# Kernel optimization log

Hardware: AMD Instinct MI355X
Metric: run time of the kernel (lower is better)

Reference implementation:

```python
import jax, jax.numpy as jnp
import numpy as np

B, S, D, H = 2, 2048, 1024, 16
DK = D // H


def setup_inputs() -> dict:
    key = jax.random.key(0)
    ks = jax.random.split(key, 12)
    scale = 1.0 / np.sqrt(D)
    inp = {
        "q": jax.random.normal(ks[0], (B, S, D), dtype=jnp.float32),
        "k": jax.random.normal(ks[1], (B, S, D), dtype=jnp.float32),
        "v": jax.random.normal(ks[2], (B, S, D), dtype=jnp.float32),
        "mask": jax.random.randint(ks[3], (B, 1, 1, S), 0, 2, dtype=jnp.int32),
        "Wq": jax.random.normal(ks[4], (D, D), dtype=jnp.float32) * scale,
        "bq": jnp.zeros((D,), dtype=jnp.float32),
        "Wk": jax.random.normal(ks[5], (D, D), dtype=jnp.float32) * scale,
        "bk": jnp.zeros((D,), dtype=jnp.float32),
        "Wv": jax.random.normal(ks[6], (D, D), dtype=jnp.float32) * scale,
        "bv": jnp.zeros((D,), dtype=jnp.float32),
        "Wo": jax.random.normal(ks[7], (D, D), dtype=jnp.float32) * scale,
        "bo": jnp.zeros((D,), dtype=jnp.float32),
    }
    return inp


def reference(q, k, v, mask, Wq, bq, Wk, bk, Wv, bv, Wo, bo):
    # Linear projections (torch nn.Linear: x @ W.T + b)
    query = q @ Wq.T + bq                      # [B,S,D]
    key = k @ Wk.T + bk
    value = v @ Wv.T + bv
    # split heads -> [B,H,S,DK]
    def split(x):
        return x.reshape(B, S, H, DK).transpose(0, 2, 1, 3)
    qh, kh, vh = split(query), split(key), split(value)
    # scaled dot-product attention with additive mask
    scores = jnp.einsum("bhqd,bhkd->bhqk", qh, kh) / jnp.sqrt(jnp.float32(DK))
    scores = jnp.where(mask == 0, jnp.float32(-1e9), scores)
    attn = jax.nn.softmax(scores, axis=-1)     # [B,H,S,S]
    out = jnp.einsum("bhqk,bhkd->bhqd", attn, vh)
    out = out.transpose(0, 2, 1, 3).reshape(B, S, D)
    return out @ Wo.T + bo
```

## Files before the change

kernel.cpp:

```cpp
#include <hip/hip_runtime.h>


constexpr int BB = 2;
constexpr int SS = 2048;
constexpr int DD = 1024;
constexpr int HH = 16;
constexpr int DKK = 64;

typedef float f32x4 __attribute__((ext_vector_type(4)));
typedef __bf16 bf16x8 __attribute__((ext_vector_type(8)));
typedef short s16x8 __attribute__((ext_vector_type(8)));
typedef short s16x4 __attribute__((ext_vector_type(4)));

#define DEV static __device__ __forceinline__

DEV f32x4 mfma16(s16x8 a, s16x8 b, f32x4 c) {
  return __builtin_amdgcn_mfma_f32_16x16x32_bf16(
      __builtin_bit_cast(bf16x8, a), __builtin_bit_cast(bf16x8, b), c, 0, 0, 0);
}

DEV void split1(float x, short& h, short& l) {
  unsigned u = __float_as_uint(x);
  h = (short)(u >> 16);
  float hf = __uint_as_float(u & 0xffff0000u);
  l = (short)(__float_as_uint(x - hf) >> 16);
}
DEV short f2bf_rne(float x) {
  unsigned u = __float_as_uint(x);
  return (short)((u + 0x7fffu + ((u >> 16) & 1u)) >> 16);
}
DEV s16x8 load8s(const short* p) { return *(const s16x8*)p; }

DEV void gld_lds16(const short* g, short* l) {
  __builtin_amdgcn_global_load_lds(
      (const __attribute__((address_space(1))) void*)g,
      (__attribute__((address_space(3))) void*)l, 16, 0, 0);
}

__global__ __launch_bounds__(256) void split_pair(const float* __restrict__ X,
                                                  short* __restrict__ H,
                                                  short* __restrict__ L) {
  int i = (blockIdx.x * 256 + threadIdx.x) * 4;
  float4 x = *(const float4*)(X + i);
  float xs[4] = {x.x, x.y, x.z, x.w};
  s16x4 h4, l4;
#pragma unroll
  for (int e = 0; e < 4; ++e) {
    short h, l;
    split1(xs[e], h, l);
    h4[e] = h;
    l4[e] = l;
  }
  *(s16x4*)(H + i) = h4;
  *(s16x4*)(L + i) = l4;
}

__global__ __launch_bounds__(256) void cast_rne(const float* __restrict__ X,
                                                short* __restrict__ Y) {
  int i = (blockIdx.x * 256 + threadIdx.x) * 4;
  float4 x = *(const float4*)(X + i);
  float xs[4] = {x.x, x.y, x.z, x.w};
  s16x4 y4;
#pragma unroll
  for (int e = 0; e < 4; ++e) y4[e] = f2bf_rne(xs[e]);
  *(s16x4*)(Y + i) = y4;
}

__global__ __launch_bounds__(256) void gemm_qk(
    const short* __restrict__ qAh, const short* __restrict__ qAl,
    const short* __restrict__ Wqh, const short* __restrict__ Wql,
    const float* __restrict__ bq, short* __restrict__ Qo,
    const short* __restrict__ kAh, const short* __restrict__ kAl,
    const short* __restrict__ Wkh, const short* __restrict__ Wkl,
    const float* __restrict__ bk, short* __restrict__ Kho,
    short* __restrict__ Klo) {
  __shared__ short lds[2][12288];

  const int tid = threadIdx.x;
  const int lane = tid & 63, wv = tid >> 6;
  const int lo16 = lane & 15, quad = lane >> 4;
  const int sel = blockIdx.x >> 9;
  const int bid = blockIdx.x & 511;
  const int m0 = (bid & 31) * 128;
  const int n0 = (bid >> 5) * 64;

  const short* Agh = sel ? kAh : qAh;
  const short* Agl = sel ? kAl : qAl;
  const short* Wgh = sel ? Wkh : Wqh;
  const short* Wgl = sel ? Wkl : Wql;
  const float* bias = sel ? bk : bq;

  f32x4 acc[2][4];
#pragma unroll
  for (int mt = 0; mt < 2; ++mt)
#pragma unroll
    for (int nt = 0; nt < 4; ++nt) acc[mt][nt] = f32x4{0.f, 0.f, 0.f, 0.f};

  const int rw = tid >> 2, qw = tid & 3;
  const int ra0 = tid >> 2, ra1 = (tid + 256) >> 2;

  auto stage = [&](int k0, int buf) {
    short* sAh = lds[buf];
    short* sAl = lds[buf] + 4096;
    short* sWh = lds[buf] + 8192;
    short* sWl = lds[buf] + 10240;
    gld_lds16(Wgh + (size_t)(n0 + rw) * DD + k0 + qw * 8, sWh + tid * 8);
    gld_lds16(Wgl + (size_t)(n0 + rw) * DD + k0 + qw * 8, sWl + tid * 8);
    gld_lds16(Agh + (size_t)(m0 + ra0) * DD + k0 + qw * 8, sAh + tid * 8);
    gld_lds16(Agh + (size_t)(m0 + ra1) * DD + k0 + qw * 8, sAh + (tid + 256) * 8);
    gld_lds16(Agl + (size_t)(m0 + ra0) * DD + k0 + qw * 8, sAl + tid * 8);
    gld_lds16(Agl + (size_t)(m0 + ra1) * DD + k0 + qw * 8, sAl + (tid + 256) * 8);
  };

  stage(0, 0);

  for (int kk = 0; kk < DD / 32; ++kk) {
    __syncthreads();
    if (kk + 1 < DD / 32) stage((kk + 1) * 32, (kk + 1) & 1);

    const short* sAh = lds[kk & 1];
    const short* sAl = lds[kk & 1] + 4096;
    const short* sWh = lds[kk & 1] + 8192;
    const short* sWl = lds[kk & 1] + 10240;

    s16x8 ah[2], al[2], wh[4], wl[4];
#pragma unroll
    for (int mt = 0; mt < 2; ++mt) {
      const int r = wv * 32 + mt * 16 + lo16;
      ah[mt] = *(const s16x8*)&sAh[r * 32 + quad * 8];
      al[mt] = *(const s16x8*)&sAl[r * 32 + quad * 8];
    }
#pragma unroll
    for (int nt = 0; nt < 4; ++nt) {
      const int r = nt * 16 + lo16;
      wh[nt] = *(const s16x8*)&sWh[r * 32 + quad * 8];
      wl[nt] = *(const s16x8*)&sWl[r * 32 + quad * 8];
    }
#pragma unroll
    for (int mt = 0; mt < 2; ++mt)
#pragma unroll
      for (int nt = 0; nt < 4; ++nt) {
        acc[mt][nt] = mfma16(ah[mt], wh[nt], acc[mt][nt]);
        acc[mt][nt] = mfma16(ah[mt], wl[nt], acc[mt][nt]);
        acc[mt][nt] = mfma16(al[mt], wh[nt], acc[mt][nt]);
      }
  }

#pragma unroll
  for (int mt = 0; mt < 2; ++mt)
#pragma unroll
    for (int nt = 0; nt < 4; ++nt) {
      const int n = n0 + nt * 16 + lo16;
      const float bv = bias[n];
#pragma unroll
      for (int r = 0; r < 4; ++r) {
        const int m = m0 + wv * 32 + mt * 16 + quad * 4 + r;
        const float val = acc[mt][nt][r] + bv;
        const int b = m >> 11, s = m & 2047;
        const int h = n >> 6, dk = n & 63;
        size_t idx = ((size_t)(b * HH + h) * SS + s) * DKK + dk;
        if (sel == 0) {
          Qo[idx] = f2bf_rne(val);
        } else {
          short hh, ll;
          split1(val, hh, ll);
          Kho[idx] = hh;
          Klo[idx] = ll;
        }
      }
    }
}

template <int SPLIT, int EPI>
__global__ __launch_bounds__(256) void gemm_tile(
    const short* __restrict__ Agh, const short* __restrict__ Agl,
    const short* __restrict__ Wgh, const short* __restrict__ Wgl,
    const float* __restrict__ bias, void* __restrict__ O1, void* __restrict__ O2) {
  __shared__ short lds[2][12288];

  const int tid = threadIdx.x;
  const int lane = tid & 63, wv = tid >> 6;
  const int lo16 = lane & 15, quad = lane >> 4;
  const int m0 = (blockIdx.x & 31) * 128;
  const int n0 = (blockIdx.x >> 5) * 64;

  f32x4 acc[2][4];
#pragma unroll
  for (int mt = 0; mt < 2; ++mt)
#pragma unroll
    for (int nt = 0; nt < 4; ++nt) acc[mt][nt] = f32x4{0.f, 0.f, 0.f, 0.f};

  const int rw = tid >> 2, qw = tid & 3;
  const int ra0 = tid >> 2, ra1 = (tid + 256) >> 2;

  auto stage = [&](int k0, int buf) {
    short* sAh = lds[buf];
    short* sAl = lds[buf] + 4096;
    short* sWh = lds[buf] + 8192;
    short* sWl = lds[buf] + 10240;
    gld_lds16(Wgh + (size_t)(n0 + rw) * DD + k0 + qw * 8, sWh + tid * 8);
    if constexpr (SPLIT)
      gld_lds16(Wgl + (size_t)(n0 + rw) * DD + k0 + qw * 8, sWl + tid * 8);
    gld_lds16(Agh + (size_t)(m0 + ra0) * DD + k0 + qw * 8, sAh + tid * 8);
    gld_lds16(Agh + (size_t)(m0 + ra1) * DD + k0 + qw * 8, sAh + (tid + 256) * 8);
    if constexpr (SPLIT) {
      gld_lds16(Agl + (size_t)(m0 + ra0) * DD + k0 + qw * 8, sAl + tid * 8);
      gld_lds16(Agl + (size_t)(m0 + ra1) * DD + k0 + qw * 8, sAl + (tid + 256) * 8);
    }
  };

  stage(0, 0);

  for (int kk = 0; kk < DD / 32; ++kk) {
    __syncthreads();
    if (kk + 1 < DD / 32) stage((kk + 1) * 32, (kk + 1) & 1);

    const short* sAh = lds[kk & 1];
    const short* sAl = lds[kk & 1] + 4096;
    const short* sWh = lds[kk & 1] + 8192;
    const short* sWl = lds[kk & 1] + 10240;

    s16x8 ah[2], al[2], wh[4], wl[4];
#pragma unroll
    for (int mt = 0; mt < 2; ++mt) {
      const int r = wv * 32 + mt * 16 + lo16;
      ah[mt] = *(const s16x8*)&sAh[r * 32 + quad * 8];
      if constexpr (SPLIT) al[mt] = *(const s16x8*)&sAl[r * 32 + quad * 8];
    }
#pragma unroll
    for (int nt = 0; nt < 4; ++nt) {
      const int r = nt * 16 + lo16;
      wh[nt] = *(const s16x8*)&sWh[r * 32 + quad * 8];
      if constexpr (SPLIT) wl[nt] = *(const s16x8*)&sWl[r * 32 + quad * 8];
    }
#pragma unroll
    for (int mt = 0; mt < 2; ++mt)
#pragma unroll
      for (int nt = 0; nt < 4; ++nt) {
        acc[mt][nt] = mfma16(ah[mt], wh[nt], acc[mt][nt]);
        if constexpr (SPLIT) {
          acc[mt][nt] = mfma16(ah[mt], wl[nt], acc[mt][nt]);
          acc[mt][nt] = mfma16(al[mt], wh[nt], acc[mt][nt]);
        }
      }
  }

#pragma unroll
  for (int mt = 0; mt < 2; ++mt)
#pragma unroll
    for (int nt = 0; nt < 4; ++nt) {
      const int n = n0 + nt * 16 + lo16;
      const float bv = bias[n];
#pragma unroll
      for (int r = 0; r < 4; ++r) {
        const int m = m0 + wv * 32 + mt * 16 + quad * 4 + r;
        const float val = acc[mt][nt][r] + bv;
        const int b = m >> 11, s = m & 2047;
        const int h = n >> 6, dk = n & 63;
        if constexpr (EPI == 1) {
          size_t idx = ((size_t)(b * HH + h) * DKK + dk) * SS + s;
          ((short*)O1)[idx] = f2bf_rne(val);
        } else {
          ((float*)O1)[(size_t)m * DD + n] = val;
        }
      }
    }
}

constexpr int PAD = 68;
constexpr int NKB = SS / 64;

__global__ __launch_bounds__(256, 2) void mha_attn(
    const short* __restrict__ Qh, const short* __restrict__ Kh,
    const short* __restrict__ Kl, const short* __restrict__ Vt,
    const int* __restrict__ mask, short* __restrict__ Ah,
    short* __restrict__ Al) {
  __shared__ short sKh[64 * PAD];
  __shared__ short sKl[64 * PAD];
  __shared__ short sV[64 * PAD];
  __shared__ short sP[4][32 * PAD];

  const int tid = threadIdx.x;
  const int lane = tid & 63, wv = tid >> 6;
  const int lo16 = lane & 15, quad = lane >> 4;
  const int bid = blockIdx.x;
  const int head = (bid & 7) * 4 + ((bid >> 3) & 3);
  const int qblk = bid >> 5;
  const int q0 = qblk * 128 + wv * 32;
  const int b = head >> 4;

  const size_t hbase = (size_t)head * SS;

  s16x8 qh[2][2];
#pragma unroll
  for (int rt = 0; rt < 2; ++rt) {
    size_t qb = (hbase + q0 + rt * 16 + lo16) * DKK + quad * 8;
#pragma unroll
    for (int c = 0; c < 2; ++c) qh[rt][c] = load8s(Qh + qb + c * 32);
  }

  f32x4 Oacc[2][4];
#pragma unroll
  for (int rt = 0; rt < 2; ++rt)
#pragma unroll
    for (int t = 0; t < 4; ++t) Oacc[rt][t] = f32x4{0.f, 0.f, 0.f, 0.f};
  float lsum[2][4];
#pragma unroll
  for (int rt = 0; rt < 2; ++rt)
#pragma unroll
    for (int r = 0; r < 4; ++r) lsum[rt][r] = 0.f;

  const int srow = tid >> 2;
  const int scol0 = (tid & 3) * 8;

  s16x8 rKh[2], rKl[2], rV[2];
#pragma unroll
  for (int i = 0; i < 2; ++i) {
    const int sc_ = scol0 + i * 32;
    rKh[i] = load8s(Kh + (hbase + srow) * DKK + sc_);
    rKl[i] = load8s(Kl + (hbase + srow) * DKK + sc_);
    rV[i] = load8s(Vt + ((size_t)head * DKK + srow) * SS + sc_);
  }

  for (int kb = 0; kb < NKB; ++kb) {
    const int k0g = kb * 64;
#pragma unroll
    for (int i = 0; i < 2; ++i) {
      const int sc_ = scol0 + i * 32;
      *(s16x8*)&sKh[srow * PAD + sc_] = rKh[i];
      *(s16x8*)&sKl[srow * PAD + sc_] = rKl[i];
      *(s16x8*)&sV[srow * PAD + sc_] = rV[i];
    }
    __syncthreads();

    if (kb + 1 < NKB) {
      const int k0n = k0g + 64;
#pragma unroll
      for (int i = 0; i < 2; ++i) {
        const int sc_ = scol0 + i * 32;
        rKh[i] = load8s(Kh + (hbase + k0n + srow) * DKK + sc_);
        rKl[i] = load8s(Kl + (hbase + k0n + srow) * DKK + sc_);
        rV[i] = load8s(Vt + ((size_t)head * DKK + srow) * SS + k0n + sc_);
      }
    }

    f32x4 sc4[2][4];
    int mv[4];
#pragma unroll
    for (int sub = 0; sub < 4; ++sub) {
      mv[sub] = mask[b * SS + k0g + sub * 16 + lo16];
      sc4[0][sub] = f32x4{0.f, 0.f, 0.f, 0.f};
      sc4[1][sub] = f32x4{0.f, 0.f, 0.f, 0.f};
      const int krow = sub * 16 + lo16;
#pragma unroll
      for (int c = 0; c < 2; ++c) {
        s16x8 kh = *(const s16x8*)&sKh[krow * PAD + c * 32 + quad * 8];
        s16x8 kl = *(const s16x8*)&sKl[krow * PAD + c * 32 + quad * 8];
#pragma unroll
        for (int rt = 0; rt < 2; ++rt) {
          sc4[rt][sub] = mfma16(qh[rt][c], kh, sc4[rt][sub]);
          sc4[rt][sub] = mfma16(qh[rt][c], kl, sc4[rt][sub]);
        }
      }
    }

#pragma unroll
    for (int rt = 0; rt < 2; ++rt)
#pragma unroll
      for (int sub = 0; sub < 4; ++sub)
#pragma unroll
        for (int r = 0; r < 4; ++r) {
          float p = __expf(sc4[rt][sub][r] * 0.125f);
          p = mv[sub] ? p : 0.f;
          lsum[rt][r] += p;
          sP[wv][(rt * 16 + quad * 4 + r) * PAD + sub * 16 + lo16] = f2bf_rne(p);
        }

    s16x8 pa[2][2];
#pragma unroll
    for (int rt = 0; rt < 2; ++rt)
#pragma unroll
      for (int c = 0; c < 2; ++c)
        pa[rt][c] = *(const s16x8*)&sP[wv][(rt * 16 + lo16) * PAD + c * 32 + quad * 8];
#pragma unroll
    for (int t = 0; t < 4; ++t)
#pragma unroll
      for (int c = 0; c < 2; ++c) {
        s16x8 vb = *(const s16x8*)&sV[(t * 16 + lo16) * PAD + c * 32 + quad * 8];
#pragma unroll
        for (int rt = 0; rt < 2; ++rt)
          Oacc[rt][t] = mfma16(pa[rt][c], vb, Oacc[rt][t]);
      }
    __syncthreads();
  }

  const int h = head & 15;
#pragma unroll
  for (int rt = 0; rt < 2; ++rt)
#pragma unroll
    for (int r = 0; r < 4; ++r) {
      float s = lsum[rt][r];
#pragma unroll
      for (int off = 1; off < 16; off <<= 1) s += __shfl_xor(s, off);
      const float rinv = 1.0f / s;
#pragma unroll
      for (int t = 0; t < 4; ++t) {
        const float val = Oacc[rt][t][r] * rinv;
        const int row = q0 + rt * 16 + quad * 4 + r;
        const int col = h * DKK + t * 16 + lo16;
        const size_t idx = ((size_t)b * SS + row) * DD + col;
        short hh, ll;
        split1(val, hh, ll);
        Ah[idx] = hh;
        Al[idx] = ll;
      }
    }
}

extern "C" void kernel_launch(void* const* d_in, const int* in_sizes, int n_in,
                              void* d_out, int out_size, void* d_ws, size_t ws_size,
                              hipStream_t stream) {
  const float* q = (const float*)d_in[0];
  const float* k = (const float*)d_in[1];
  const float* v = (const float*)d_in[2];
  const int* mask = (const int*)d_in[3];
  const float* Wq = (const float*)d_in[4];
  const float* bq = (const float*)d_in[5];
  const float* Wk = (const float*)d_in[6];
  const float* bk = (const float*)d_in[7];
  const float* Wv = (const float*)d_in[8];
  const float* bv = (const float*)d_in[9];
  const float* Wo = (const float*)d_in[10];
  const float* bo = (const float*)d_in[11];

  char* ws = (char*)d_ws;
  size_t off = 0;
  auto take = [&](size_t bytes) {
    char* p = ws + off;
    off += (bytes + 255) & ~(size_t)255;
    return p;
  };
  const size_t WE = (size_t)DD * DD;
  const size_t TE = (size_t)BB * SS * DD;

  short* Wqh = (short*)take(WE * 2);
  short* Wql = (short*)take(WE * 2);
  short* Wkh = (short*)take(WE * 2);
  short* Wkl = (short*)take(WE * 2);
  short* Wvh = (short*)take(WE * 2);
  short* Woh = (short*)take(WE * 2);
  short* Wol = (short*)take(WE * 2);
  short* qH = (short*)take(TE * 2);
  short* qL = (short*)take(TE * 2);
  short* kH = (short*)take(TE * 2);
  short* kL = (short*)take(TE * 2);
  short* Qh = (short*)take(TE * 2);
  short* Kh = (short*)take(TE * 2);
  short* Kl = (short*)take(TE * 2);
  (void)ws_size;
  short* vH = qH;
  short* Vt = qL;
  short* aH = kH;
  short* aL = kL;

  split_pair<<<1024, 256, 0, stream>>>(Wq, Wqh, Wql);
  split_pair<<<1024, 256, 0, stream>>>(Wk, Wkh, Wkl);
  split_pair<<<1024, 256, 0, stream>>>(Wo, Woh, Wol);
  cast_rne<<<1024, 256, 0, stream>>>(Wv, Wvh);

  split_pair<<<4096, 256, 0, stream>>>(q, qH, qL);
  split_pair<<<4096, 256, 0, stream>>>(k, kH, kL);

  gemm_qk<<<1024, 256, 0, stream>>>(qH, qL, Wqh, Wql, bq, Qh,
                                    kH, kL, Wkh, Wkl, bk, Kh, Kl);

  cast_rne<<<4096, 256, 0, stream>>>(v, vH);
  gemm_tile<0, 1><<<512, 256, 0, stream>>>(vH, nullptr, Wvh, nullptr, bv, Vt, nullptr);

  mha_attn<<<512, 256, 0, stream>>>(Qh, Kh, Kl, Vt, mask, aH, aL);

  gemm_tile<1, 2><<<512, 256, 0, stream>>>(aH, aL, Woh, Wol, bo, d_out, nullptr);
}
```

Measured before the change: 332.2 us.

## Load GEMM A operands directly to registers and swizzle W LDS tiles

In both projection GEMM kernels, the A-operand fragments are now loaded straight from global memory into registers with one-step register prefetch, since each wave owns its own A rows and needs no LDS sharing. Only the W tiles are staged through double-buffered LDS, which shrinks shared memory per block from 48KB to 16KB. W tiles use an XOR swizzle of the 8-element column chunks to reduce LDS bank conflicts on the MFMA fragment reads. The trade-off is more live registers and uncoalesced-ish per-lane global loads of A, in exchange for higher occupancy and less LDS traffic.

```diff
diff --git a/kernel.cpp b/kernel.cpp
--- a/kernel.cpp
+++ b/kernel.cpp
@@ -74,7 +74,7 @@
     const short* __restrict__ Wkh, const short* __restrict__ Wkl,
     const float* __restrict__ bk, short* __restrict__ Kho,
     short* __restrict__ Klo) {
-  __shared__ short lds[2][12288];
+  __shared__ short lds[2][4096];
 
   const int tid = threadIdx.x;
   const int lane = tid & 63, wv = tid >> 6;
@@ -96,45 +96,41 @@
 #pragma unroll
     for (int nt = 0; nt < 4; ++nt) acc[mt][nt] = f32x4{0.f, 0.f, 0.f, 0.f};
 
-  const int rw = tid >> 2, qw = tid & 3;
-  const int ra0 = tid >> 2, ra1 = (tid + 256) >> 2;
-
-  auto stage = [&](int k0, int buf) {
-    short* sAh = lds[buf];
-    short* sAl = lds[buf] + 4096;
-    short* sWh = lds[buf] + 8192;
-    short* sWl = lds[buf] + 10240;
-    gld_lds16(Wgh + (size_t)(n0 + rw) * DD + k0 + qw * 8, sWh + tid * 8);
-    gld_lds16(Wgl + (size_t)(n0 + rw) * DD + k0 + qw * 8, sWl + tid * 8);
-    gld_lds16(Agh + (size_t)(m0 + ra0) * DD + k0 + qw * 8, sAh + tid * 8);
-    gld_lds16(Agh + (size_t)(m0 + ra1) * DD + k0 + qw * 8, sAh + (tid + 256) * 8);
-    gld_lds16(Agl + (size_t)(m0 + ra0) * DD + k0 + qw * 8, sAl + tid * 8);
-    gld_lds16(Agl + (size_t)(m0 + ra1) * DD + k0 + qw * 8, sAl + (tid + 256) * 8);
-  };
-
-  stage(0, 0);
+  const int wr = tid >> 2, wp = tid & 3;
+  const size_t wsrc = (size_t)(n0 + wr) * DD + (wp ^ ((wr >> 1) & 3)) * 8;
+  const int pq = quad ^ ((lo16 >> 1) & 3);
+
+  const size_t a0 = (size_t)(m0 + wv * 32 + lo16) * DD + quad * 8;
+  const size_t a1 = a0 + (size_t)16 * DD;
+
+  s16x8 ah[2], al[2];
+  ah[0] = load8s(Agh + a0);
+  ah[1] = load8s(Agh + a1);
+  al[0] = load8s(Agl + a0);
+  al[1] = load8s(Agl + a1);
+  gld_lds16(Wgh + wsrc, &lds[0][tid * 8]);
+  gld_lds16(Wgl + wsrc, &lds[0][2048 + tid * 8]);
 
   for (int kk = 0; kk < DD / 32; ++kk) {
     __syncthreads();
-    if (kk + 1 < DD / 32) stage((kk + 1) * 32, (kk + 1) & 1);
-
-    const short* sAh = lds[kk & 1];
-    const short* sAl = lds[kk & 1] + 4096;
-    const short* sWh = lds[kk & 1] + 8192;
-    const short* sWl = lds[kk & 1] + 10240;
-
-    s16x8 ah[2], al[2], wh[4], wl[4];
-#pragma unroll
-    for (int mt = 0; mt < 2; ++mt) {
-      const int r = wv * 32 + mt * 16 + lo16;
-      ah[mt] = *(const s16x8*)&sAh[r * 32 + quad * 8];
-      al[mt] = *(const s16x8*)&sAl[r * 32 + quad * 8];
-    }
+    s16x8 ahn[2], aln[2];
+    const bool more = (kk + 1 < DD / 32);
+    if (more) {
+      const int k1 = (kk + 1) * 32;
+      gld_lds16(Wgh + wsrc + k1, &lds[(kk + 1) & 1][tid * 8]);
+      gld_lds16(Wgl + wsrc + k1, &lds[(kk + 1) & 1][2048 + tid * 8]);
+      ahn[0] = load8s(Agh + a0 + k1);
+      ahn[1] = load8s(Agh + a1 + k1);
+      aln[0] = load8s(Agl + a0 + k1);
+      aln[1] = load8s(Agl + a1 + k1);
+    }
+    const short* sWh = lds[kk & 1];
+    const short* sWl = lds[kk & 1] + 2048;
+    s16x8 wh[4], wl[4];
 #pragma unroll
     for (int nt = 0; nt < 4; ++nt) {
-      const int r = nt * 16 + lo16;
-      wh[nt] = *(const s16x8*)&sWh[r * 32 + quad * 8];
-      wl[nt] = *(const s16x8*)&sWl[r * 32 + quad * 8];
+      wh[nt] = *(const s16x8*)&sWh[(nt * 16 + lo16) * 32 + pq * 8];
+      wl[nt] = *(const s16x8*)&sWl[(nt * 16 + lo16) * 32 + pq * 8];
     }
 #pragma unroll
     for (int mt = 0; mt < 2; ++mt)
@@ -144,6 +140,12 @@
         acc[mt][nt] = mfma16(ah[mt], wl[nt], acc[mt][nt]);
         acc[mt][nt] = mfma16(al[mt], wh[nt], acc[mt][nt]);
       }
+    if (more) {
+      ah[0] = ahn[0];
+      ah[1] = ahn[1];
+      al[0] = aln[0];
+      al[1] = aln[1];
+    }
   }
 
 #pragma unroll
@@ -176,7 +178,7 @@
     const short* __restrict__ Agh, const short* __restrict__ Agl,
     const short* __restrict__ Wgh, const short* __restrict__ Wgl,
     const float* __restrict__ bias, void* __restrict__ O1, void* __restrict__ O2) {
-  __shared__ short lds[2][12288];
+  __shared__ short lds[2][4096];
 
   const int tid = threadIdx.x;
   const int lane = tid & 63, wv = tid >> 6;
@@ -190,48 +192,47 @@
 #pragma unroll
     for (int nt = 0; nt < 4; ++nt) acc[mt][nt] = f32x4{0.f, 0.f, 0.f, 0.f};
 
-  const int rw = tid >> 2, qw = tid & 3;
-  const int ra0 = tid >> 2, ra1 = (tid + 256) >> 2;
-
-  auto stage = [&](int k0, int buf) {
-    short* sAh = lds[buf];
-    short* sAl = lds[buf] + 4096;
-    short* sWh = lds[buf] + 8192;
-    short* sWl = lds[buf] + 10240;
-    gld_lds16(Wgh + (size_t)(n0 + rw) * DD + k0 + qw * 8, sWh + tid * 8);
-    if constexpr (SPLIT)
-      gld_lds16(Wgl + (size_t)(n0 + rw) * DD + k0 + qw * 8, sWl + tid * 8);
-    gld_lds16(Agh + (size_t)(m0 + ra0) * DD + k0 + qw * 8, sAh + tid * 8);
-    gld_lds16(Agh + (size_t)(m0 + ra1) * DD + k0 + qw * 8, sAh + (tid + 256) * 8);
-    if constexpr (SPLIT) {
-      gld_lds16(Agl + (size_t)(m0 + ra0) * DD + k0 + qw * 8, sAl + tid * 8);
-      gld_lds16(Agl + (size_t)(m0 + ra1) * DD + k0 + qw * 8, sAl + (tid + 256) * 8);
-    }
-  };
-
-  stage(0, 0);
+  const int wr = tid >> 2, wp = tid & 3;
+  const size_t wsrc = (size_t)(n0 + wr) * DD + (wp ^ ((wr >> 1) & 3)) * 8;
+  const int pq = quad ^ ((lo16 >> 1) & 3);
+
+  const size_t a0 = (size_t)(m0 + wv * 32 + lo16) * DD + quad * 8;
+  const size_t a1 = a0 + (size_t)16 * DD;
+
+  s16x8 ah[2], al[2];
+  ah[0] = load8s(Agh + a0);
+  ah[1] = load8s(Agh + a1);
+  if constexpr (SPLIT) {
+    al[0] = load8s(Agl + a0);
+    al[1] = load8s(Agl + a1);
+  }
+  gld_lds16(Wgh + wsrc, &lds[0][tid * 8]);
+  if constexpr (SPLIT) gld_lds16(Wgl + wsrc, &lds[0][2048 + tid * 8]);
 
   for (int kk = 0; kk < DD / 32; ++kk) {
     __syncthreads();
-    if (kk + 1 < DD / 32) stage((kk + 1) * 32, (kk + 1) & 1);
-
-    const short* sAh = lds[kk & 1];
-    const short* sAl = lds[kk & 1] + 4096;
-    const short* sWh = lds[kk & 1] + 8192;
-    const short* sWl = lds[kk & 1] + 10240;
-
-    s16x8 ah[2], al[2], wh[4], wl[4];
-#pragma unroll
-    for (int mt = 0; mt < 2; ++mt) {
-      const int r = wv * 32 + mt * 16 + lo16;
-      ah[mt] = *(const s16x8*)&sAh[r * 32 + quad * 8];
-      if constexpr (SPLIT) al[mt] = *(const s16x8*)&sAl[r * 32 + quad * 8];
-    }
+    s16x8 ahn[2], aln[2];
+    const bool more = (kk + 1 < DD / 32);
+    if (more) {
+      const int k1 = (kk + 1) * 32;
+      gld_lds16(Wgh + wsrc + k1, &lds[(kk + 1) & 1][tid * 8]);
+      if constexpr (SPLIT)
+        gld_lds16(Wgl + wsrc + k1, &lds[(kk + 1) & 1][2048 + tid * 8]);
+      ahn[0] = load8s(Agh + a0 + k1);
+      ahn[1] = load8s(Agh + a1 + k1);
+      if constexpr (SPLIT) {
+        aln[0] = load8s(Agl + a0 + k1);
+        aln[1] = load8s(Agl + a1 + k1);
+      }
+    }
+    const short* sWh = lds[kk & 1];
+    const short* sWl = lds[kk & 1] + 2048;
+    s16x8 wh[4], wl[4];
 #pragma unroll
     for (int nt = 0; nt < 4; ++nt) {
-      const int r = nt * 16 + lo16;
-      wh[nt] = *(const s16x8*)&sWh[r * 32 + quad * 8];
-      if constexpr (SPLIT) wl[nt] = *(const s16x8*)&sWl[r * 32 + quad * 8];
+      wh[nt] = *(const s16x8*)&sWh[(nt * 16 + lo16) * 32 + pq * 8];
+      if constexpr (SPLIT)
+        wl[nt] = *(const s16x8*)&sWl[(nt * 16 + lo16) * 32 + pq * 8];
     }
 #pragma unroll
     for (int mt = 0; mt < 2; ++mt)
@@ -243,6 +244,14 @@
           acc[mt][nt] = mfma16(al[mt], wh[nt], acc[mt][nt]);
         }
       }
+    if (more) {
+      ah[0] = ahn[0];
+      ah[1] = ahn[1];
+      if constexpr (SPLIT) {
+        al[0] = aln[0];
+        al[1] = aln[1];
+      }
+    }
   }
 
 #pragma unroll
```

New measurement: 360.3 us. 8.5% more time.
